# Kernel tuning notes

Measured on AMD Instinct MI355X. Metric: run time of the kernel, lower is better.

Reference implementation:

```python
import jax, jax.numpy as jnp
import numpy as np

NUM_EMBED = 1024
NUM_HEADS = 16
BLOCK_SIZE = 2048


def setup_inputs() -> dict:
    key = jax.random.key(0)
    k1, k2, k3, k4, k5 = jax.random.split(key, 5)
    C = NUM_EMBED
    s = 1.0 / np.sqrt(C)
    x = jax.random.normal(k1, (2, BLOCK_SIZE, C), dtype=jnp.float32)
    # nn.Linear params: weight (out,in), bias (out,)
    w_attn = jax.random.uniform(k2, (3 * C, C), minval=-s, maxval=s, dtype=jnp.float32)
    b_attn = jax.random.uniform(k3, (3 * C,), minval=-s, maxval=s, dtype=jnp.float32)
    w_proj = jax.random.uniform(k4, (C, C), minval=-s, maxval=s, dtype=jnp.float32)
    b_proj = jax.random.uniform(k5, (C,), minval=-s, maxval=s, dtype=jnp.float32)
    return {"x": x, "w_attn": w_attn, "b_attn": b_attn, "w_proj": w_proj, "b_proj": b_proj}


def reference(x, w_attn, b_attn, w_proj, b_proj):
    B, T, C = x.shape
    H = NUM_HEADS
    D = C // H
    kqv = jnp.einsum('btc,oc->bto', x, w_attn) + b_attn  # (B,T,3C)
    # Original code splits as K, Q, V in that order.
    K, Q, V = jnp.split(kqv, 3, axis=2)
    K = K.reshape(B, T, H, D).transpose(0, 2, 1, 3)  # (B,H,T,D)
    Q = Q.reshape(B, T, H, D).transpose(0, 2, 1, 3)
    V = V.reshape(B, T, H, D).transpose(0, 2, 1, 3)
    aff = jnp.einsum('bhqd,bhkd->bhqk', Q, K) * (D ** -0.5)  # (B,H,T,T)
    causal = jnp.tril(jnp.ones((T, T), dtype=bool))
    aff = jnp.where(causal[None, None], aff, jnp.float32(-jnp.inf))
    wei = jax.nn.softmax(aff, axis=-1)
    attn = jnp.einsum('bhqk,bhkd->bhqd', wei, V)
    attn = attn.transpose(0, 2, 1, 3).reshape(B, T, C)
    out = jnp.einsum('btc,oc->bto', attn, w_proj) + b_proj
    return out
```

## Files before the change

kernel.cpp:

```cpp
#include <hip/hip_runtime.h>
#include <hip/hip_bf16.h>
#include <cstdint>

typedef __attribute__((ext_vector_type(8))) short bf16x8;
typedef __attribute__((ext_vector_type(4))) float f32x4;
typedef __attribute__((ext_vector_type(16))) float f32x16;
typedef __attribute__((ext_vector_type(4))) uint16_t u16x4;

__device__ __forceinline__ uint16_t f2b(float f) {
  union { float f; uint32_t i; } v; v.f = f;
  return (uint16_t)((v.i + 0x7FFFu + ((v.i >> 16) & 1u)) >> 16);
}

__device__ __forceinline__ uint32_t pkbf(float a, float b) {
  union { __hip_bfloat162 h2; uint32_t u; } c;
  c.h2 = __float22bfloat162_rn(make_float2(a, b));
  return c.u;
}

#define GLDS16(g, l) __builtin_amdgcn_global_load_lds( \
    (const __attribute__((address_space(1))) void*)(g), \
    (__attribute__((address_space(3))) void*)(l), 16, 0, 0)

__global__ __launch_bounds__(256) void cvt_all(
    const float* __restrict__ x, const float* __restrict__ wa, const float* __restrict__ wp,
    uint16_t* __restrict__ xb, uint16_t* __restrict__ wab, uint16_t* __restrict__ wpb) {
  const int i = (blockIdx.x * 256 + threadIdx.x) * 4;
  const float* src; uint16_t* dst; int off;
  if (i < 4194304)      { src = x;  dst = xb;  off = i; }
  else if (i < 7340032) { src = wa; dst = wab; off = i - 4194304; }
  else                  { src = wp; dst = wpb; off = i - 7340032; }
  const float4 v = *(const float4*)(src + off);
  u16x4 o;
  o.x = f2b(v.x); o.y = f2b(v.y); o.z = f2b(v.z); o.w = f2b(v.w);
  *(u16x4*)(dst + off) = o;
}

template <int BM, bool OUT_BF16>
__global__ __launch_bounds__(256) void gemm_bt_bias(
    const uint16_t* __restrict__ A, const uint16_t* __restrict__ B,
    const float* __restrict__ bias, void* __restrict__ Cv,
    int M, int N, int K) {
  constexpr int MI = BM / 32;
  constexpr int CA = BM / 16;
  constexpr int CPW = (2 * (CA + 8)) / 4;
  constexpr int CT_PITCH = OUT_BF16 ? 72 : 68;
  constexpr size_t CT_BYTES = (size_t)4 * (BM / 2) * CT_PITCH * (OUT_BF16 ? 2 : 4);
  constexpr size_t ST_BYTES = (size_t)(2 * (BM * 32 + 4096)) * 2;
  constexpr size_t LB = CT_BYTES > ST_BYTES ? CT_BYTES : ST_BYTES;
  __shared__ alignas(16) unsigned char ldsb[LB];
  uint16_t* lds = (uint16_t*)ldsb;
  const int offB0 = BM * 32;
  const int offA1 = BM * 32 + 4096;
  const int offB1 = 2 * BM * 32 + 4096;

  const int tid = threadIdx.x;
  const int wave = tid >> 6, lane = tid & 63;
  const int q4 = lane >> 4, l16 = lane & 15;
  const int wm = wave >> 1, wn = wave & 1;
  const long blockM = (long)blockIdx.y * BM;
  const long blockN = (long)blockIdx.x * 128;

  f32x4 acc[MI][4] = {};

  for (int k0 = 0; k0 < K; k0 += 64) {
#pragma unroll
    for (int c = 0; c < CPW; ++c) {
      const int id = c * 4 + wave;
      const uint16_t* mat; long rowBase; int a, kk, off;
      if (id < CA)               { mat = A; rowBase = blockM; a = id;            kk = k0;      off = 0; }
      else if (id < CA + 8)      { mat = B; rowBase = blockN; a = id - CA;       kk = k0;      off = offB0; }
      else if (id < 2 * CA + 8)  { mat = A; rowBase = blockM; a = id - CA - 8;   kk = k0 + 32; off = offA1; }
      else                       { mat = B; rowBase = blockN; a = id - 2*CA - 8; kk = k0 + 32; off = offB1; }
      const int flat = a * 64 + lane;
      const int row = flat >> 2, seg = flat & 3;
      GLDS16(mat + (rowBase + row) * (long)K + kk + seg * 8, lds + off + a * 512);
    }
    __syncthreads();
#pragma unroll
    for (int h = 0; h < 2; ++h) {
      const uint16_t* Ah = lds + (h ? offA1 : 0);
      const uint16_t* Bh = lds + (h ? offB1 : offB0);
      bf16x8 af[MI], bfr[4];
#pragma unroll
      for (int i = 0; i < MI; ++i)
        af[i] = *(const bf16x8*)&Ah[(wm * (BM / 2) + i * 16 + l16) * 32 + q4 * 8];
#pragma unroll
      for (int j = 0; j < 4; ++j)
        bfr[j] = *(const bf16x8*)&Bh[(wn * 64 + j * 16 + l16) * 32 + q4 * 8];
#pragma unroll
      for (int i = 0; i < MI; ++i)
#pragma unroll
        for (int j = 0; j < 4; ++j)
          acc[i][j] = __builtin_amdgcn_mfma_f32_16x16x32_bf16(af[i], bfr[j], acc[i][j], 0, 0, 0);
    }
    __syncthreads();
  }

  if (OUT_BF16) {
    uint16_t* ct = lds + wave * (BM / 2) * 72;
#pragma unroll
    for (int j = 0; j < 4; ++j) {
      const float bv = bias[blockN + wn * 64 + j * 16 + l16];
#pragma unroll
      for (int i = 0; i < MI; ++i)
#pragma unroll
        for (int r = 0; r < 4; ++r)
          ct[(i * 16 + q4 * 4 + r) * 72 + j * 16 + l16] = f2b(acc[i][j][r] + bv);
    }
    __syncthreads();
    uint16_t* Cb = (uint16_t*)Cv;
#pragma unroll
    for (int st = 0; st < BM / 16; ++st) {
      const int flat = st * 64 + lane;
      const int row = flat >> 3, seg = flat & 7;
      const bf16x8 v = *(const bf16x8*)&ct[row * 72 + seg * 8];
      *(bf16x8*)&Cb[(blockM + wm * (BM / 2) + row) * (long)N + blockN + wn * 64 + seg * 8] = v;
    }
  } else {
    float* ct = (float*)ldsb + wave * (BM / 2) * 68;
#pragma unroll
    for (int j = 0; j < 4; ++j) {
      const float bv = bias[blockN + wn * 64 + j * 16 + l16];
#pragma unroll
      for (int i = 0; i < MI; ++i)
#pragma unroll
        for (int r = 0; r < 4; ++r)
          ct[(i * 16 + q4 * 4 + r) * 68 + j * 16 + l16] = acc[i][j][r] + bv;
    }
    __syncthreads();
    float* Cb = (float*)Cv;
#pragma unroll
    for (int st = 0; st < BM / 8; ++st) {
      const int flat = st * 64 + lane;
      const int row = flat >> 4, seg = flat & 15;
      const f32x4 v = *(const f32x4*)&ct[row * 68 + seg * 4];
      *(f32x4*)&Cb[(blockM + wm * (BM / 2) + row) * (long)N + blockN + wn * 64 + seg * 4] = v;
    }
  }
}

__global__ __launch_bounds__(256, 2) void attn_flash(
    const uint16_t* __restrict__ kqv, uint16_t* __restrict__ attn) {
  constexpr int T = 2048, C = 1024, C3 = 3072;
  __shared__ alignas(16) unsigned char ldsb[35840];
  uint16_t* KP = (uint16_t*)ldsb;
  uint16_t* Vt = (uint16_t*)(ldsb + 18432);
  uint32_t* VtW = (uint32_t*)(ldsb + 18432);
  float* mlb  = (float*)ldsb;
  float* obuf = (float*)(ldsb + 1024);

  const int tid = threadIdx.x;
  const int wave = tid >> 6, lane = tid & 63;
  const int l32 = lane & 31, hh = lane >> 5;
  const int pairi = blockIdx.x >> 5, bh = blockIdx.x & 31;
  const int b = bh >> 4, h = bh & 15;
  const size_t base = (size_t)b * T * C3;
  const int hD = h * 64;
  const int lr = lane >> 3, kch = lane & 7;
  const float sc = 0.125f * 1.4426950408889634f;

  for (int ss = 0; ss < 2; ++ss) {
    const int qb = ss ? pairi : 31 - pairi;
    const int dd = qb * 64 + 63 - wave * 32;
    const int nktw = (dd < 0) ? 0 : ((dd >> 7) + 1);

    bf16x8 qf[2][4];
#pragma unroll
    for (int qc = 0; qc < 2; ++qc)
#pragma unroll
      for (int m = 0; m < 4; ++m)
        qf[qc][m] = *(const bf16x8*)&kqv[base + (size_t)(qb * 64 + qc * 32 + l32) * C3 + C + hD + m * 16 + hh * 8];

    f32x16 o[2][2] = {};
    float m_i[2] = {-1e30f, -1e30f}, l_i[2] = {0.f, 0.f};

    bf16x8 pk[4], pv0[2], pv1[2];
    if (nktw > 0) {
      const int kb0 = wave * 32;
#pragma unroll
      for (int rr = 0; rr < 4; ++rr)
        pk[rr] = *(const bf16x8*)&kqv[base + (size_t)(kb0 + rr * 8 + lr) * C3 + hD + kch * 8];
#pragma unroll
      for (int s2 = 0; s2 < 2; ++s2) {
        const size_t gg = base + (size_t)(kb0 + 2 * (s2 * 8 + lr)) * C3 + 2 * C + hD + kch * 8;
        pv0[s2] = *(const bf16x8*)&kqv[gg];
        pv1[s2] = *(const bf16x8*)&kqv[gg + C3];
      }
    }

    for (int kt = 0; kt < nktw; ++kt) {
      const int key0 = kt * 128 + wave * 32;
#pragma unroll
      for (int rr = 0; rr < 4; ++rr)
        *(bf16x8*)&KP[(wave * 32 + rr * 8 + lr) * 72 + kch * 8] = pk[rr];
#pragma unroll
      for (int s2 = 0; s2 < 2; ++s2) {
        const int colw = (wave * 16 + s2 * 8 + lr + 8 * kch) & 63;
        const uint32_t* a0 = (const uint32_t*)&pv0[s2];
        const uint32_t* a1 = (const uint32_t*)&pv1[s2];
#pragma unroll
        for (int i = 0; i < 8; ++i) {
          const uint32_t w = (i & 1)
              ? __builtin_amdgcn_perm(a1[i >> 1], a0[i >> 1], 0x07060302u)
              : __builtin_amdgcn_perm(a1[i >> 1], a0[i >> 1], 0x05040100u);
          VtW[(kch * 8 + i) * 68 + colw] = w;
        }
      }
      if (kt + 1 < nktw) {
        const int kb2 = (kt + 1) * 128 + wave * 32;
#pragma unroll
        for (int rr = 0; rr < 4; ++rr)
          pk[rr] = *(const bf16x8*)&kqv[base + (size_t)(kb2 + rr * 8 + lr) * C3 + hD + kch * 8];
#pragma unroll
        for (int s2 = 0; s2 < 2; ++s2) {
          const size_t gg = base + (size_t)(kb2 + 2 * (s2 * 8 + lr)) * C3 + 2 * C + hD + kch * 8;
          pv0[s2] = *(const bf16x8*)&kqv[gg];
          pv1[s2] = *(const bf16x8*)&kqv[gg + C3];
        }
      }

      bf16x8 kf[4];
#pragma unroll
      for (int m = 0; m < 4; ++m)
        kf[m] = *(const bf16x8*)&KP[(wave * 32 + l32) * 72 + m * 16 + hh * 8];

#pragma unroll
      for (int qc = 0; qc < 2; ++qc) {
        if (key0 > qb * 64 + qc * 32 + 31) continue;
        f32x16 z = {};
#pragma unroll
        for (int m = 0; m < 4; ++m)
          z = __builtin_amdgcn_mfma_f32_32x32x16_bf16(kf[m], qf[qc][m], z, 0, 0, 0);
        if (key0 + 31 > qb * 64 + qc * 32) {
          const int qg = qb * 64 + qc * 32 + l32;
#pragma unroll
          for (int r = 0; r < 16; ++r) {
            const int kg = key0 + (r & 3) + 8 * (r >> 2) + 4 * hh;
            if (kg > qg) z[r] = -1e30f;
          }
        }
        float mloc = -1e30f;
#pragma unroll
        for (int r = 0; r < 16; ++r) mloc = fmaxf(mloc, z[r]);
        mloc = fmaxf(mloc, __shfl_xor(mloc, 32, 64));
        const float pm = fmaxf(mloc * sc, -3.0e4f);
        if (__any(pm - m_i[qc] > 8.0f)) {
          const float mnew = fmaxf(m_i[qc], pm);
          const float alpha = exp2f(m_i[qc] - mnew);
#pragma unroll
          for (int r = 0; r < 16; ++r) {
            const float ar = __shfl(alpha, (r & 3) + 8 * (r >> 2) + 4 * hh, 64);
            o[qc][0][r] *= ar;
            o[qc][1][r] *= ar;
          }
          l_i[qc] *= alpha;
          m_i[qc] = mnew;
        }
        float rs = 0.f;
#pragma unroll
        for (int r = 0; r < 16; ++r) {
          const float pe = exp2f(fmaf(z[r], sc, -m_i[qc]));
          z[r] = pe;
          rs += pe;
        }
        rs += __shfl_xor(rs, 32, 64);
        l_i[qc] += rs;

        uint32_t x0 = pkbf(z[0], z[1]),   x1 = pkbf(z[2], z[3]);
        uint32_t y0 = pkbf(z[4], z[5]),   y1 = pkbf(z[6], z[7]);
        uint32_t x2 = pkbf(z[8], z[9]),   x3 = pkbf(z[10], z[11]);
        uint32_t y2 = pkbf(z[12], z[13]), y3 = pkbf(z[14], z[15]);
        const uint32_t s0 = hh ? x0 : y0, s1 = hh ? x1 : y1;
        const uint32_t s2 = hh ? x2 : y2, s3 = hh ? x3 : y3;
        const uint32_t t0 = __shfl_xor(s0, 32, 64), t1 = __shfl_xor(s1, 32, 64);
        const uint32_t t2 = __shfl_xor(s2, 32, 64), t3 = __shfl_xor(s3, 32, 64);
#pragma unroll
        for (int cc = 0; cc < 2; ++cc) {
          union { bf16x8 v; uint32_t w[4]; } pa;
          if (cc == 0) {
            pa.w[0] = hh ? t0 : x0; pa.w[1] = hh ? t1 : x1;
            pa.w[2] = hh ? y0 : t0; pa.w[3] = hh ? y1 : t1;
          } else {
            pa.w[0] = hh ? t2 : x2; pa.w[1] = hh ? t3 : x3;
            pa.w[2] = hh ? y2 : t2; pa.w[3] = hh ? y3 : t3;
          }
#pragma unroll
          for (int db = 0; db < 2; ++db) {
            const int d = db * 32 + l32;
            const int col = (wave * 32 + cc * 16 + hh * 8 + 16 * (d >> 3)) & 127;
            const bf16x8 vf = *(const bf16x8*)&Vt[d * 136 + col];
            o[qc][db] = __builtin_amdgcn_mfma_f32_32x32x16_bf16(pa.v, vf, o[qc][db], 0, 0, 0);
          }
        }
      }
    }

#pragma unroll
    for (int qc = 0; qc < 2; ++qc) {
      __syncthreads();
      if (hh == 0) {
        mlb[wave * 64 + l32] = m_i[qc];
        mlb[wave * 64 + 32 + l32] = l_i[qc];
      }
#pragma unroll
      for (int r = 0; r < 16; ++r) {
        const int ql = (r & 3) + 8 * (r >> 2) + 4 * hh;
        const int bw = wave * 2112 + ql * 66 + l32;
        obuf[bw] = o[qc][0][r];
        obuf[bw + 32] = o[qc][1][r];
      }
      __syncthreads();
      float mw[4], lw[4];
#pragma unroll
      for (int w = 0; w < 4; ++w) {
        mw[w] = mlb[w * 64 + l32];
        lw[w] = mlb[w * 64 + 32 + l32];
      }
      const float M = fmaxf(fmaxf(mw[0], mw[1]), fmaxf(mw[2], mw[3]));
      float L = 0.f, ww[4];
#pragma unroll
      for (int w = 0; w < 4; ++w) { ww[w] = exp2f(mw[w] - M); L += lw[w] * ww[w]; }
      const float Li = 1.0f / L;
      const int cb = wave * 2 + hh;
      float acc[8] = {};
#pragma unroll
      for (int w = 0; w < 4; ++w)
#pragma unroll
        for (int p = 0; p < 4; ++p) {
          const float2 v = *(const float2*)&obuf[w * 2112 + l32 * 66 + cb * 8 + p * 2];
          acc[2 * p]     += v.x * ww[w];
          acc[2 * p + 1] += v.y * ww[w];
        }
      union { bf16x8 v; uint32_t w4[4]; } ov;
#pragma unroll
      for (int p = 0; p < 4; ++p)
        ov.w4[p] = pkbf(acc[2 * p] * Li, acc[2 * p + 1] * Li);
      *(bf16x8*)&attn[((size_t)b * T + qb * 64 + qc * 32 + l32) * C + hD + cb * 8] = ov.v;
    }
    __syncthreads();
  }
}

extern "C" void kernel_launch(void* const* d_in, const int* in_sizes, int n_in,
                              void* d_out, int out_size, void* d_ws, size_t ws_size,
                              hipStream_t stream) {
  const float* x      = (const float*)d_in[0];
  const float* w_attn = (const float*)d_in[1];
  const float* b_attn = (const float*)d_in[2];
  const float* w_proj = (const float*)d_in[3];
  const float* b_proj = (const float*)d_in[4];
  float* out = (float*)d_out;

  uint16_t* xb    = (uint16_t*)d_ws;
  uint16_t* wab   = xb  + (size_t)4096 * 1024;
  uint16_t* wpb   = wab + (size_t)3072 * 1024;
  uint16_t* kqv   = wpb + (size_t)1024 * 1024;
  uint16_t* attnb = kqv + (size_t)4096 * 3072;

  dim3 blk(256, 1, 1);
  hipLaunchKernelGGL(cvt_all, dim3(8192), blk, 0, stream, x, w_attn, w_proj, xb, wab, wpb);

  hipLaunchKernelGGL((gemm_bt_bias<128, true>), dim3(3072 / 128, 4096 / 128, 1), blk, 0, stream,
                     xb, wab, b_attn, (void*)kqv, 4096, 3072, 1024);
  hipLaunchKernelGGL(attn_flash, dim3(512, 1, 1), blk, 0, stream, kqv, attnb);
  hipLaunchKernelGGL((gemm_bt_bias<64, false>), dim3(1024 / 128, 4096 / 64, 1), blk, 0, stream,
                     attnb, wpb, b_proj, (void*)out, 4096, 1024, 1024);
}
```

Before: 193.0 us.

## Launch one attention block per query tile and use permlane32 swap for P exchange

Measured after the change: 192.4 us. Within noise of the previous version (-0.3%).

```diff
diff --git a/kernel.cpp b/kernel.cpp
--- a/kernel.cpp
+++ b/kernel.cpp
@@ -153,192 +153,189 @@
   const int tid = threadIdx.x;
   const int wave = tid >> 6, lane = tid & 63;
   const int l32 = lane & 31, hh = lane >> 5;
-  const int pairi = blockIdx.x >> 5, bh = blockIdx.x & 31;
+  const int sidx = blockIdx.x >> 5, bh = blockIdx.x & 31;
   const int b = bh >> 4, h = bh & 15;
   const size_t base = (size_t)b * T * C3;
   const int hD = h * 64;
   const int lr = lane >> 3, kch = lane & 7;
   const float sc = 0.125f * 1.4426950408889634f;
 
-  for (int ss = 0; ss < 2; ++ss) {
-    const int qb = ss ? pairi : 31 - pairi;
-    const int dd = qb * 64 + 63 - wave * 32;
-    const int nktw = (dd < 0) ? 0 : ((dd >> 7) + 1);
-
-    bf16x8 qf[2][4];
-#pragma unroll
-    for (int qc = 0; qc < 2; ++qc)
-#pragma unroll
-      for (int m = 0; m < 4; ++m)
-        qf[qc][m] = *(const bf16x8*)&kqv[base + (size_t)(qb * 64 + qc * 32 + l32) * C3 + C + hD + m * 16 + hh * 8];
-
-    f32x16 o[2][2] = {};
-    float m_i[2] = {-1e30f, -1e30f}, l_i[2] = {0.f, 0.f};
-
-    bf16x8 pk[4], pv0[2], pv1[2];
-    if (nktw > 0) {
-      const int kb0 = wave * 32;
+  const int qb = 31 - sidx;
+  const int dd = qb * 64 + 63 - wave * 32;
+  const int nktw = (dd < 0) ? 0 : ((dd >> 7) + 1);
+
+  bf16x8 qf[2][4];
+#pragma unroll
+  for (int qc = 0; qc < 2; ++qc)
+#pragma unroll
+    for (int m = 0; m < 4; ++m)
+      qf[qc][m] = *(const bf16x8*)&kqv[base + (size_t)(qb * 64 + qc * 32 + l32) * C3 + C + hD + m * 16 + hh * 8];
+
+  f32x16 o[2][2] = {};
+  float m_i[2] = {-1e30f, -1e30f}, l_i[2] = {0.f, 0.f};
+
+  bf16x8 pk[4], pv0[2], pv1[2];
+  if (nktw > 0) {
+    const int kb0 = wave * 32;
+#pragma unroll
+    for (int rr = 0; rr < 4; ++rr)
+      pk[rr] = *(const bf16x8*)&kqv[base + (size_t)(kb0 + rr * 8 + lr) * C3 + hD + kch * 8];
+#pragma unroll
+    for (int s2 = 0; s2 < 2; ++s2) {
+      const size_t gg = base + (size_t)(kb0 + 2 * (s2 * 8 + lr)) * C3 + 2 * C + hD + kch * 8;
+      pv0[s2] = *(const bf16x8*)&kqv[gg];
+      pv1[s2] = *(const bf16x8*)&kqv[gg + C3];
+    }
+  }
+
+  for (int kt = 0; kt < nktw; ++kt) {
+    const int key0 = kt * 128 + wave * 32;
+#pragma unroll
+    for (int rr = 0; rr < 4; ++rr)
+      *(bf16x8*)&KP[(wave * 32 + rr * 8 + lr) * 72 + kch * 8] = pk[rr];
+#pragma unroll
+    for (int s2 = 0; s2 < 2; ++s2) {
+      const int colw = (wave * 16 + s2 * 8 + lr + 8 * kch) & 63;
+      const uint32_t* a0 = (const uint32_t*)&pv0[s2];
+      const uint32_t* a1 = (const uint32_t*)&pv1[s2];
+#pragma unroll
+      for (int i = 0; i < 8; ++i) {
+        const uint32_t w = (i & 1)
+            ? __builtin_amdgcn_perm(a1[i >> 1], a0[i >> 1], 0x07060302u)
+            : __builtin_amdgcn_perm(a1[i >> 1], a0[i >> 1], 0x05040100u);
+        VtW[(kch * 8 + i) * 68 + colw] = w;
+      }
+    }
+    if (kt + 1 < nktw) {
+      const int kb2 = (kt + 1) * 128 + wave * 32;
 #pragma unroll
       for (int rr = 0; rr < 4; ++rr)
-        pk[rr] = *(const bf16x8*)&kqv[base + (size_t)(kb0 + rr * 8 + lr) * C3 + hD + kch * 8];
+        pk[rr] = *(const bf16x8*)&kqv[base + (size_t)(kb2 + rr * 8 + lr) * C3 + hD + kch * 8];
 #pragma unroll
       for (int s2 = 0; s2 < 2; ++s2) {
-        const size_t gg = base + (size_t)(kb0 + 2 * (s2 * 8 + lr)) * C3 + 2 * C + hD + kch * 8;
+        const size_t gg = base + (size_t)(kb2 + 2 * (s2 * 8 + lr)) * C3 + 2 * C + hD + kch * 8;
         pv0[s2] = *(const bf16x8*)&kqv[gg];
         pv1[s2] = *(const bf16x8*)&kqv[gg + C3];
       }
     }
 
-    for (int kt = 0; kt < nktw; ++kt) {
-      const int key0 = kt * 128 + wave * 32;
-#pragma unroll
-      for (int rr = 0; rr < 4; ++rr)
-        *(bf16x8*)&KP[(wave * 32 + rr * 8 + lr) * 72 + kch * 8] = pk[rr];
-#pragma unroll
-      for (int s2 = 0; s2 < 2; ++s2) {
-        const int colw = (wave * 16 + s2 * 8 + lr + 8 * kch) & 63;
-        const uint32_t* a0 = (const uint32_t*)&pv0[s2];
-        const uint32_t* a1 = (const uint32_t*)&pv1[s2];
-#pragma unroll
-        for (int i = 0; i < 8; ++i) {
-          const uint32_t w = (i & 1)
-              ? __builtin_amdgcn_perm(a1[i >> 1], a0[i >> 1], 0x07060302u)
-              : __builtin_amdgcn_perm(a1[i >> 1], a0[i >> 1], 0x05040100u);
-          VtW[(kch * 8 + i) * 68 + colw] = w;
+    bf16x8 kf[4];
+#pragma unroll
+    for (int m = 0; m < 4; ++m)
+      kf[m] = *(const bf16x8*)&KP[(wave * 32 + l32) * 72 + m * 16 + hh * 8];
+
+#pragma unroll
+    for (int qc = 0; qc < 2; ++qc) {
+      if (key0 > qb * 64 + qc * 32 + 31) continue;
+      f32x16 z = {};
+#pragma unroll
+      for (int m = 0; m < 4; ++m)
+        z = __builtin_amdgcn_mfma_f32_32x32x16_bf16(kf[m], qf[qc][m], z, 0, 0, 0);
+      if (key0 + 31 > qb * 64 + qc * 32) {
+        const int qg = qb * 64 + qc * 32 + l32;
+#pragma unroll
+        for (int r = 0; r < 16; ++r) {
+          const int kg = key0 + (r & 3) + 8 * (r >> 2) + 4 * hh;
+          if (kg > qg) z[r] = -1e30f;
         }
       }
-      if (kt + 1 < nktw) {
-        const int kb2 = (kt + 1) * 128 + wave * 32;
-#pragma unroll
-        for (int rr = 0; rr < 4; ++rr)
-          pk[rr] = *(const bf16x8*)&kqv[base + (size_t)(kb2 + rr * 8 + lr) * C3 + hD + kch * 8];
-#pragma unroll
-        for (int s2 = 0; s2 < 2; ++s2) {
-          const size_t gg = base + (size_t)(kb2 + 2 * (s2 * 8 + lr)) * C3 + 2 * C + hD + kch * 8;
-          pv0[s2] = *(const bf16x8*)&kqv[gg];
-          pv1[s2] = *(const bf16x8*)&kqv[gg + C3];
+      float t8[8];
+#pragma unroll
+      for (int r = 0; r < 8; ++r) t8[r] = fmaxf(z[r], z[r + 8]);
+#pragma unroll
+      for (int r = 0; r < 4; ++r) t8[r] = fmaxf(t8[r], t8[r + 4]);
+      float mloc = fmaxf(fmaxf(t8[0], t8[1]), fmaxf(t8[2], t8[3]));
+      mloc = fmaxf(mloc, __shfl_xor(mloc, 32, 64));
+      const float pm = fmaxf(mloc * sc, -3.0e4f);
+      if (__any(pm - m_i[qc] > 8.0f)) {
+        const float mnew = fmaxf(m_i[qc], pm);
+        const float alpha = exp2f(m_i[qc] - mnew);
+#pragma unroll
+        for (int r = 0; r < 16; ++r) {
+          const float ar = __shfl(alpha, (r & 3) + 8 * (r >> 2) + 4 * hh, 64);
+          o[qc][0][r] *= ar;
+          o[qc][1][r] *= ar;
         }
-      }
-
-      bf16x8 kf[4];
-#pragma unroll
-      for (int m = 0; m < 4; ++m)
-        kf[m] = *(const bf16x8*)&KP[(wave * 32 + l32) * 72 + m * 16 + hh * 8];
-
-#pragma unroll
-      for (int qc = 0; qc < 2; ++qc) {
-        if (key0 > qb * 64 + qc * 32 + 31) continue;
-        f32x16 z = {};
-#pragma unroll
-        for (int m = 0; m < 4; ++m)
-          z = __builtin_amdgcn_mfma_f32_32x32x16_bf16(kf[m], qf[qc][m], z, 0, 0, 0);
-        if (key0 + 31 > qb * 64 + qc * 32) {
-          const int qg = qb * 64 + qc * 32 + l32;
-#pragma unroll
-          for (int r = 0; r < 16; ++r) {
-            const int kg = key0 + (r & 3) + 8 * (r >> 2) + 4 * hh;
-            if (kg > qg) z[r] = -1e30f;
-          }
+        l_i[qc] *= alpha;
+        m_i[qc] = mnew;
+      }
+#pragma unroll
+      for (int r = 0; r < 16; ++r)
+        z[r] = exp2f(fmaf(z[r], sc, -m_i[qc]));
+      float s8[8];
+#pragma unroll
+      for (int r = 0; r < 8; ++r) s8[r] = z[r] + z[r + 8];
+#pragma unroll
+      for (int r = 0; r < 4; ++r) s8[r] += s8[r + 4];
+      float rs = (s8[0] + s8[1]) + (s8[2] + s8[3]);
+      rs += __shfl_xor(rs, 32, 64);
+      l_i[qc] += rs;
+
+      uint32_t x0 = pkbf(z[0], z[1]),   x1 = pkbf(z[2], z[3]);
+      uint32_t y0 = pkbf(z[4], z[5]),   y1 = pkbf(z[6], z[7]);
+      uint32_t x2 = pkbf(z[8], z[9]),   x3 = pkbf(z[10], z[11]);
+      uint32_t y2 = pkbf(z[12], z[13]), y3 = pkbf(z[14], z[15]);
+      asm volatile("v_permlane32_swap_b32 %0, %1" : "+v"(x0), "+v"(y0));
+      asm volatile("v_permlane32_swap_b32 %0, %1" : "+v"(x1), "+v"(y1));
+      asm volatile("v_permlane32_swap_b32 %0, %1" : "+v"(x2), "+v"(y2));
+      asm volatile("v_permlane32_swap_b32 %0, %1" : "+v"(x3), "+v"(y3));
+#pragma unroll
+      for (int cc = 0; cc < 2; ++cc) {
+        union { bf16x8 v; uint32_t w[4]; } pa;
+        if (cc == 0) { pa.w[0] = x0; pa.w[1] = x1; pa.w[2] = y0; pa.w[3] = y1; }
+        else         { pa.w[0] = x2; pa.w[1] = x3; pa.w[2] = y2; pa.w[3] = y3; }
+#pragma unroll
+        for (int db = 0; db < 2; ++db) {
+          const int d = db * 32 + l32;
+          const int col = (wave * 32 + cc * 16 + hh * 8 + 16 * (d >> 3)) & 127;
+          const bf16x8 vf = *(const bf16x8*)&Vt[d * 136 + col];
+          o[qc][db] = __builtin_amdgcn_mfma_f32_32x32x16_bf16(pa.v, vf, o[qc][db], 0, 0, 0);
         }
-        float mloc = -1e30f;
-#pragma unroll
-        for (int r = 0; r < 16; ++r) mloc = fmaxf(mloc, z[r]);
-        mloc = fmaxf(mloc, __shfl_xor(mloc, 32, 64));
-        const float pm = fmaxf(mloc * sc, -3.0e4f);
-        if (__any(pm - m_i[qc] > 8.0f)) {
-          const float mnew = fmaxf(m_i[qc], pm);
-          const float alpha = exp2f(m_i[qc] - mnew);
-#pragma unroll
-          for (int r = 0; r < 16; ++r) {
-            const float ar = __shfl(alpha, (r & 3) + 8 * (r >> 2) + 4 * hh, 64);
-            o[qc][0][r] *= ar;
-            o[qc][1][r] *= ar;
-          }
-          l_i[qc] *= alpha;
-          m_i[qc] = mnew;
-        }
-        float rs = 0.f;
-#pragma unroll
-        for (int r = 0; r < 16; ++r) {
-          const float pe = exp2f(fmaf(z[r], sc, -m_i[qc]));
-          z[r] = pe;
-          rs += pe;
-        }
-        rs += __shfl_xor(rs, 32, 64);
-        l_i[qc] += rs;
-
-        uint32_t x0 = pkbf(z[0], z[1]),   x1 = pkbf(z[2], z[3]);
-        uint32_t y0 = pkbf(z[4], z[5]),   y1 = pkbf(z[6], z[7]);
-        uint32_t x2 = pkbf(z[8], z[9]),   x3 = pkbf(z[10], z[11]);
-        uint32_t y2 = pkbf(z[12], z[13]), y3 = pkbf(z[14], z[15]);
-        const uint32_t s0 = hh ? x0 : y0, s1 = hh ? x1 : y1;
-        const uint32_t s2 = hh ? x2 : y2, s3 = hh ? x3 : y3;
-        const uint32_t t0 = __shfl_xor(s0, 32, 64), t1 = __shfl_xor(s1, 32, 64);
-        const uint32_t t2 = __shfl_xor(s2, 32, 64), t3 = __shfl_xor(s3, 32, 64);
-#pragma unroll
-        for (int cc = 0; cc < 2; ++cc) {
-          union { bf16x8 v; uint32_t w[4]; } pa;
-          if (cc == 0) {
-            pa.w[0] = hh ? t0 : x0; pa.w[1] = hh ? t1 : x1;
-            pa.w[2] = hh ? y0 : t0; pa.w[3] = hh ? y1 : t1;
-          } else {
-            pa.w[0] = hh ? t2 : x2; pa.w[1] = hh ? t3 : x3;
-            pa.w[2] = hh ? y2 : t2; pa.w[3] = hh ? y3 : t3;
-          }
-#pragma unroll
-          for (int db = 0; db < 2; ++db) {
-            const int d = db * 32 + l32;
-            const int col = (wave * 32 + cc * 16 + hh * 8 + 16 * (d >> 3)) & 127;
-            const bf16x8 vf = *(const bf16x8*)&Vt[d * 136 + col];
-            o[qc][db] = __builtin_amdgcn_mfma_f32_32x32x16_bf16(pa.v, vf, o[qc][db], 0, 0, 0);
-          }
-        }
-      }
-    }
-
-#pragma unroll
-    for (int qc = 0; qc < 2; ++qc) {
-      __syncthreads();
-      if (hh == 0) {
-        mlb[wave * 64 + l32] = m_i[qc];
-        mlb[wave * 64 + 32 + l32] = l_i[qc];
-      }
-#pragma unroll
-      for (int r = 0; r < 16; ++r) {
-        const int ql = (r & 3) + 8 * (r >> 2) + 4 * hh;
-        const int bw = wave * 2112 + ql * 66 + l32;
-        obuf[bw] = o[qc][0][r];
-        obuf[bw + 32] = o[qc][1][r];
-      }
-      __syncthreads();
-      float mw[4], lw[4];
-#pragma unroll
-      for (int w = 0; w < 4; ++w) {
-        mw[w] = mlb[w * 64 + l32];
-        lw[w] = mlb[w * 64 + 32 + l32];
-      }
-      const float M = fmaxf(fmaxf(mw[0], mw[1]), fmaxf(mw[2], mw[3]));
-      float L = 0.f, ww[4];
-#pragma unroll
-      for (int w = 0; w < 4; ++w) { ww[w] = exp2f(mw[w] - M); L += lw[w] * ww[w]; }
-      const float Li = 1.0f / L;
-      const int cb = wave * 2 + hh;
-      float acc[8] = {};
-#pragma unroll
-      for (int w = 0; w < 4; ++w)
-#pragma unroll
-        for (int p = 0; p < 4; ++p) {
-          const float2 v = *(const float2*)&obuf[w * 2112 + l32 * 66 + cb * 8 + p * 2];
-          acc[2 * p]     += v.x * ww[w];
-          acc[2 * p + 1] += v.y * ww[w];
-        }
-      union { bf16x8 v; uint32_t w4[4]; } ov;
-#pragma unroll
-      for (int p = 0; p < 4; ++p)
-        ov.w4[p] = pkbf(acc[2 * p] * Li, acc[2 * p + 1] * Li);
-      *(bf16x8*)&attn[((size_t)b * T + qb * 64 + qc * 32 + l32) * C + hD + cb * 8] = ov.v;
-    }
-    __syncthreads();
+      }
+    }
+  }
+
+#pragma unroll
+  for (int qc = 0; qc < 2; ++qc) {
+    __syncthreads();
+    if (hh == 0) {
+      mlb[wave * 64 + l32] = m_i[qc];
+      mlb[wave * 64 + 32 + l32] = l_i[qc];
+    }
+#pragma unroll
+    for (int r = 0; r < 16; ++r) {
+      const int ql = (r & 3) + 8 * (r >> 2) + 4 * hh;
+      const int bw = wave * 2112 + ql * 66 + l32;
+      obuf[bw] = o[qc][0][r];
+      obuf[bw + 32] = o[qc][1][r];
+    }
+    __syncthreads();
+    float mw[4], lw[4];
+#pragma unroll
+    for (int w = 0; w < 4; ++w) {
+      mw[w] = mlb[w * 64 + l32];
+      lw[w] = mlb[w * 64 + 32 + l32];
+    }
+    const float M = fmaxf(fmaxf(mw[0], mw[1]), fmaxf(mw[2], mw[3]));
+    float L = 0.f, ww[4];
+#pragma unroll
+    for (int w = 0; w < 4; ++w) { ww[w] = exp2f(mw[w] - M); L += lw[w] * ww[w]; }
+    const float Li = 1.0f / L;
+    const int cb = wave * 2 + hh;
+    float acc[8] = {};
+#pragma unroll
+    for (int w = 0; w < 4; ++w)
+#pragma unroll
+      for (int p = 0; p < 4; ++p) {
+        const float2 v = *(const float2*)&obuf[w * 2112 + l32 * 66 + cb * 8 + p * 2];
+        acc[2 * p]     += v.x * ww[w];
+        acc[2 * p + 1] += v.y * ww[w];
+      }
+    union { bf16x8 v; uint32_t w4[4]; } ov;
+#pragma unroll
+    for (int p = 0; p < 4; ++p)
+      ov.w4[p] = pkbf(acc[2 * p] * Li, acc[2 * p + 1] * Li);
+    *(bf16x8*)&attn[((size_t)b * T + qb * 64 + qc * 32 + l32) * C + hD + cb * 8] = ov.v;
   }
 }
 
@@ -363,7 +360,7 @@
 
   hipLaunchKernelGGL((gemm_bt_bias<128, true>), dim3(3072 / 128, 4096 / 128, 1), blk, 0, stream,
                      xb, wab, b_attn, (void*)kqv, 4096, 3072, 1024);
-  hipLaunchKernelGGL(attn_flash, dim3(512, 1, 1), blk, 0, stream, kqv, attnb);
+  hipLaunchKernelGGL(attn_flash, dim3(1024, 1, 1), blk, 0, stream, kqv, attnb);
   hipLaunchKernelGGL((gemm_bt_bias<64, false>), dim3(1024 / 128, 4096 / 64, 1), blk, 0, stream,
                      attnb, wpb, b_proj, (void*)out, 4096, 1024, 1024);
 }
```
